# Kernel optimization log

Hardware: AMD Instinct MI355X
Metric: run time of the kernel (lower is better)

Reference implementation:

```python
import jax, jax.numpy as jnp
import numpy as np

T, B = 128, 256          # frames, batch (free dims)
C_IN = 201               # in_features
KD = 3                   # keypoint_dimensionality
NK = C_IN // KD          # 67 keypoints = attention seq len
E = 8                    # d_pose_embed
H = 2                    # heads
DH = E // H              # head dim = 4
L = 12                   # encoder layers
FF = 2 * E               # 16
OUT = 128                # output_size
EPS = 1e-5


def setup_inputs() -> dict:
    key = jax.random.key(0)
    ks = jax.random.split(key, 12)
    s = 0.1
    return {
        "pose_clip": jax.random.normal(ks[0], (T, B, C_IN), jnp.float32),
        "embed_w": jax.random.normal(ks[1], (E, KD), jnp.float32) * s,
        "embed_b": jax.random.normal(ks[2], (E,), jnp.float32) * s,
        "in_proj_w": jax.random.normal(ks[3], (L, 3 * E, E), jnp.float32) * s,
        "in_proj_b": jax.random.normal(ks[4], (L, 3 * E), jnp.float32) * s,
        "attn_out_w": jax.random.normal(ks[5], (L, E, E), jnp.float32) * s,
        "attn_out_b": jax.random.normal(ks[6], (L, E), jnp.float32) * s,
        "ff1_w": jax.random.normal(ks[7], (L, FF, E), jnp.float32) * s,
        "ff1_b": jax.random.normal(ks[8], (L, FF), jnp.float32) * s,
        "ff2_w": jax.random.normal(ks[9], (L, E, FF), jnp.float32) * s,
        "ff2_b": jax.random.normal(ks[10], (L, E), jnp.float32) * s,
        "ln1_g": jnp.ones((L, E), jnp.float32),
        "ln1_b": jnp.zeros((L, E), jnp.float32),
        "ln2_g": jnp.ones((L, E), jnp.float32),
        "ln2_b": jnp.zeros((L, E), jnp.float32),
        "out_w": jax.random.normal(ks[11], (OUT, NK * E), jnp.float32) * s,
        "out_b": jnp.zeros((OUT,), jnp.float32),
    }


def _ln(x, g, b):
    m = jnp.mean(x, axis=-1, keepdims=True)
    v = jnp.mean(jnp.square(x - m), axis=-1, keepdims=True)
    return (x - m) * jax.lax.rsqrt(v + EPS) * g + b


def _encoder(x, layer_params):
    # x: [S, N, E]; post-LN TransformerEncoderLayer, relu activation, no dropout (eval)
    def step(h, p):
        ipw, ipb, aow, aob, f1w, f1b, f2w, f2b, g1, b1, g2, b2 = p
        S, N, _ = h.shape
        qkv = h @ ipw.T + ipb                      # [S, N, 3E]
        q, k, v = jnp.split(qkv, 3, axis=-1)
        q = q.reshape(S, N, H, DH)
        k = k.reshape(S, N, H, DH)
        v = v.reshape(S, N, H, DH)
        scores = jnp.einsum('snhd,tnhd->nhst', q, k) / np.sqrt(DH).astype(h.dtype)
        attn = jax.nn.softmax(scores, axis=-1)
        o = jnp.einsum('nhst,tnhd->snhd', attn, v).reshape(S, N, E)
        o = o @ aow.T + aob
        h = _ln(h + o, g1, b1)
        ff = jax.nn.relu(h @ f1w.T + f1b) @ f2w.T + f2b
        h = _ln(h + ff, g2, b2)
        return h, None
    x, _ = jax.lax.scan(step, x, layer_params)
    return x


def reference(pose_clip, embed_w, embed_b, in_proj_w, in_proj_b, attn_out_w,
              attn_out_b, ff1_w, ff1_b, ff2_w, ff2_b, ln1_g, ln1_b, ln2_g,
              ln2_b, out_w, out_b):
    t, b, c = pose_clip.shape
    nk = c // KD
    # [t,b,c] -> [t*b, nk, 3] -> [nk, t*b, 3]  (seq=keypoints, batch=t*b)
    x = pose_clip.reshape(t * b, nk, KD).transpose(1, 0, 2)
    x = x @ embed_w.T + embed_b                    # [nk, t*b, E]
    layer_params = (in_proj_w, in_proj_b, attn_out_w, attn_out_b,
                    ff1_w, ff1_b, ff2_w, ff2_b, ln1_g, ln1_b, ln2_g, ln2_b)
    x = _encoder(x, layer_params)
    x = x.transpose(1, 0, 2).reshape(t, b, nk * E)  # [t, b, 536]
    return jnp.tanh(x @ out_w.T + out_b)            # [t, b, 128]
```

## Files before the change

kernel.cpp:

```cpp
#include <hip/hip_runtime.h>
#include <math.h>

#define NTOT 32768
#define CIN  201
#define S    67
#define E    8
#define H    2
#define L    12
#define FF   16
#define OUTC 128
#define KF   536
#define EPB  7
#define LPE  34
#define THREADS 256
#define NPAIR 34

typedef float v2f __attribute__((ext_vector_type(2)));

#if __has_builtin(__builtin_amdgcn_exp2f)
#define EXP2F(x) __builtin_amdgcn_exp2f(x)
#else
#define EXP2F(x) exp2f(x)
#endif
#if __has_builtin(__builtin_amdgcn_rcpf)
#define RCPF(x) __builtin_amdgcn_rcpf(x)
#else
#define RCPF(x) (1.0f/(x))
#endif
#if __has_builtin(__builtin_amdgcn_rsqf)
#define RSQF(x) __builtin_amdgcn_rsqf(x)
#else
#define RSQF(x) rsqrtf(x)
#endif

#define QSCALE 0.7213475204444817f

__device__ __forceinline__ v2f sp(float x) { return (v2f){x, x}; }

__device__ __forceinline__ void ln8p(v2f* x, const float* __restrict__ gg,
                                     const float* __restrict__ bb) {
    v2f m = {0.f, 0.f};
    #pragma unroll
    for (int e = 0; e < E; ++e) m += x[e];
    m *= 0.125f;
    v2f v = {0.f, 0.f};
    #pragma unroll
    for (int e = 0; e < E; ++e) { v2f d = x[e] - m; v += d * d; }
    v *= 0.125f;
    v2f rs;
    rs.x = RSQF(v.x + 1e-5f);
    rs.y = RSQF(v.y + 1e-5f);
    #pragma unroll
    for (int e = 0; e < E; ++e) x[e] = (x[e] - m) * rs * sp(gg[e]) + sp(bb[e]);
}

__global__ __launch_bounds__(THREADS, 5)
void enc_kernel(const float* __restrict__ pose,
                const float* __restrict__ ew,  const float* __restrict__ ebias,
                const float* __restrict__ ipw, const float* __restrict__ ipb,
                const float* __restrict__ aow, const float* __restrict__ aob,
                const float* __restrict__ f1w, const float* __restrict__ f1b,
                const float* __restrict__ f2w, const float* __restrict__ f2b,
                const float* __restrict__ g1,  const float* __restrict__ b1,
                const float* __restrict__ g2,  const float* __restrict__ b2,
                float* __restrict__ xf)
{
    __shared__ float4 KA[EPB * H][NPAIR];
    __shared__ float4 KB[EPB * H][NPAIR];
    __shared__ float4 VA[EPB * H][NPAIR];
    __shared__ float4 VB[EPB * H][NPAIR];

    const int lid = threadIdx.x;
    const int g   = lid / LPE;
    const int j   = lid - g * LPE;
    const int n   = blockIdx.x * EPB + g;
    const bool active = (g < EPB) && (n < NTOT);
    const bool pad = (j == LPE - 1);
    const int r0 = 2 * j;

    v2f xr[E];
    if (active) {
        const float* p0 = pose + (size_t)n * CIN + 3 * r0;
        const float* p1 = pad ? p0 : (p0 + 3);
        v2f c0 = {p0[0], p1[0]};
        v2f c1 = {p0[1], p1[1]};
        v2f c2 = {p0[2], p1[2]};
        #pragma unroll
        for (int e = 0; e < E; ++e)
            xr[e] = sp(ebias[e]) + c0 * sp(ew[e*3+0]) + c1 * sp(ew[e*3+1])
                                 + c2 * sp(ew[e*3+2]);
    }

    #pragma unroll 1
    for (int l = 0; l < L; ++l) {
        const float* W  = ipw + l * 192;
        const float* Bq = ipb + l * 24;

        v2f qp[E];
        if (active) {
            v2f qkv[24];
            #pragma unroll
            for (int jo = 0; jo < 24; ++jo) {
                v2f a = sp(Bq[jo]);
                #pragma unroll
                for (int e = 0; e < E; ++e) a += xr[e] * sp(W[jo*8 + e]);
                qkv[jo] = a;
            }
            #pragma unroll
            for (int c = 0; c < E; ++c) qp[c] = qkv[c] * QSCALE;
            if (pad) {
                #pragma unroll
                for (int c = 8; c < 24; ++c) qkv[c].y = 0.f;
            }
            #pragma unroll
            for (int h = 0; h < H; ++h) {
                const int gh = g*2 + h;
                KA[gh][j] = make_float4(qkv[8+4*h+0].x, qkv[8+4*h+0].y,
                                        qkv[8+4*h+1].x, qkv[8+4*h+1].y);
                KB[gh][j] = make_float4(qkv[8+4*h+2].x, qkv[8+4*h+2].y,
                                        qkv[8+4*h+3].x, qkv[8+4*h+3].y);
                VA[gh][j] = make_float4(qkv[16+4*h+0].x, qkv[16+4*h+0].y,
                                        qkv[16+4*h+1].x, qkv[16+4*h+1].y);
                VB[gh][j] = make_float4(qkv[16+4*h+2].x, qkv[16+4*h+2].y,
                                        qkv[16+4*h+3].x, qkv[16+4*h+3].y);
            }
        }
        __syncthreads();

        if (active) {
            v2f os[E];
            #pragma unroll
            for (int h = 0; h < H; ++h) {
                const int gh = g*2 + h;
                const float4* pKA = KA[gh];
                const float4* pKB = KB[gh];
                const float4* pVA = VA[gh];
                const float4* pVB = VB[gh];
                const v2f q0l = sp(qp[4*h+0].x), q0h = sp(qp[4*h+0].y);
                const v2f q1l = sp(qp[4*h+1].x), q1h = sp(qp[4*h+1].y);
                const v2f q2l = sp(qp[4*h+2].x), q2h = sp(qp[4*h+2].y);
                const v2f q3l = sp(qp[4*h+3].x), q3h = sp(qp[4*h+3].y);
                v2f ls0 = {0.f,0.f}, ls1 = {0.f,0.f};
                v2f oc00={0.f,0.f}, oc01={0.f,0.f}, oc02={0.f,0.f}, oc03={0.f,0.f};
                v2f oc10={0.f,0.f}, oc11={0.f,0.f}, oc12={0.f,0.f}, oc13={0.f,0.f};
                #pragma unroll
                for (int i = 0; i < NPAIR; ++i) {
                    float4 ka = pKA[i], kb = pKB[i];
                    float4 va = pVA[i], vb = pVB[i];
                    v2f kx = *(const v2f*)&ka.x, ky = *(const v2f*)&ka.z;
                    v2f kz = *(const v2f*)&kb.x, kw = *(const v2f*)&kb.z;
                    v2f sc0 = q0l*kx + q1l*ky + q2l*kz + q3l*kw;
                    v2f sc1 = q0h*kx + q1h*ky + q2h*kz + q3h*kw;
                    v2f e0, e1;
                    e0.x = EXP2F(sc0.x);  e0.y = EXP2F(sc0.y);
                    e1.x = EXP2F(sc1.x);  e1.y = EXP2F(sc1.y);
                    ls0 += e0;  ls1 += e1;
                    v2f v0 = *(const v2f*)&va.x, v1 = *(const v2f*)&va.z;
                    v2f v2 = *(const v2f*)&vb.x, v3 = *(const v2f*)&vb.z;
                    oc00 += e0*v0; oc01 += e0*v1; oc02 += e0*v2; oc03 += e0*v3;
                    oc10 += e1*v0; oc11 += e1*v1; oc12 += e1*v2; oc13 += e1*v3;
                }
                float l0 = ls0.x + ls0.y - 1.0f;
                float l1 = ls1.x + ls1.y - 1.0f;
                float i0 = RCPF(l0), i1 = RCPF(l1);
                os[4*h+0] = (v2f){(oc00.x+oc00.y)*i0, (oc10.x+oc10.y)*i1};
                os[4*h+1] = (v2f){(oc01.x+oc01.y)*i0, (oc11.x+oc11.y)*i1};
                os[4*h+2] = (v2f){(oc02.x+oc02.y)*i0, (oc12.x+oc12.y)*i1};
                os[4*h+3] = (v2f){(oc03.x+oc03.y)*i0, (oc13.x+oc13.y)*i1};
            }

            {
                const float* WA = aow + l*64;
                const float* BA = aob + l*8;
                #pragma unroll
                for (int e = 0; e < E; ++e) {
                    v2f a = sp(BA[e]);
                    #pragma unroll
                    for (int e2 = 0; e2 < E; ++e2) a += os[e2] * sp(WA[e*8 + e2]);
                    xr[e] += a;
                }
            }
            ln8p(xr, g1 + l*E, b1 + l*E);

            {
                const float* W1 = f1w + l*128;
                const float* B1 = f1b + l*16;
                const float* W2 = f2w + l*128;
                const float* B2 = f2b + l*8;
                v2f t1[FF];
                #pragma unroll
                for (int f = 0; f < FF; ++f) {
                    v2f a = sp(B1[f]);
                    #pragma unroll
                    for (int e = 0; e < E; ++e) a += xr[e] * sp(W1[f*8 + e]);
                    a.x = fmaxf(a.x, 0.f);
                    a.y = fmaxf(a.y, 0.f);
                    t1[f] = a;
                }
                #pragma unroll
                for (int e = 0; e < E; ++e) {
                    v2f a = sp(B2[e]);
                    #pragma unroll
                    for (int f = 0; f < FF; ++f) a += t1[f] * sp(W2[e*16 + f]);
                    xr[e] += a;
                }
            }
            ln8p(xr, g2 + l*E, b2 + l*E);
        }
        __syncthreads();
    }

    if (active) {
        float* dst = xf + (size_t)n * KF + r0 * E;
        *(float4*)(dst + 0) = make_float4(xr[0].x, xr[1].x, xr[2].x, xr[3].x);
        *(float4*)(dst + 4) = make_float4(xr[4].x, xr[5].x, xr[6].x, xr[7].x);
        if (!pad) {
            *(float4*)(dst + 8)  = make_float4(xr[0].y, xr[1].y, xr[2].y, xr[3].y);
            *(float4*)(dst + 12) = make_float4(xr[4].y, xr[5].y, xr[6].y, xr[7].y);
        }
    }
}

__global__ void tr_kernel(const float* __restrict__ ow, float* __restrict__ wt)
{
    int i = blockIdx.x * 256 + threadIdx.x;
    if (i < OUTC * KF) {
        int c = i / KF, k = i - c * KF;
        wt[k * OUTC + c] = ow[i];
    }
}

__global__ __launch_bounds__(256, 4)
void out_kernel(const float* __restrict__ xf, const float* __restrict__ wt,
                const float* __restrict__ ob, float* __restrict__ out)
{
    __shared__ float Xs[32][68];
    const int lid = threadIdx.x;
    const int tx  = lid & 31;
    const int ty  = lid >> 5;
    const int n0  = blockIdx.x * 32;

    float acc[4][4] = {};

    #pragma unroll 1
    for (int kc = 0; kc < 9; ++kc) {
        const int kb = kc * 64;
        const int kw = (kc < 8) ? 64 : 24;
        __syncthreads();
        const int nvec = 32 * (kw >> 2);
        for (int i = lid; i < nvec; i += 256) {
            int r = i / (kw >> 2), kq = i - r * (kw >> 2);
            *(float4*)&Xs[r][kq*4] =
                *(const float4*)&xf[(size_t)(n0 + r) * KF + kb + kq*4];
        }
        __syncthreads();
        #pragma unroll 4
        for (int k = 0; k < kw; ++k) {
            float4 w4 = *(const float4*)&wt[(size_t)(kb + k) * OUTC + tx*4];
            #pragma unroll
            for (int i = 0; i < 4; ++i) {
                float x = Xs[ty*4 + i][k];
                acc[i][0] += x*w4.x; acc[i][1] += x*w4.y;
                acc[i][2] += x*w4.z; acc[i][3] += x*w4.w;
            }
        }
    }

    const float4 bb = *(const float4*)&ob[tx*4];
    #pragma unroll
    for (int i = 0; i < 4; ++i) {
        int r = n0 + ty*4 + i;
        float4 v;
        v.x = tanhf(acc[i][0] + bb.x);
        v.y = tanhf(acc[i][1] + bb.y);
        v.z = tanhf(acc[i][2] + bb.z);
        v.w = tanhf(acc[i][3] + bb.w);
        *(float4*)(out + (size_t)r * OUTC + tx*4) = v;
    }
}

extern "C" void kernel_launch(void* const* d_in, const int* in_sizes, int n_in,
                              void* d_out, int out_size, void* d_ws, size_t ws_size,
                              hipStream_t stream) {
    (void)in_sizes; (void)n_in; (void)out_size; (void)ws_size;
    const float* pose = (const float*)d_in[0];
    const float* ew   = (const float*)d_in[1];
    const float* eb   = (const float*)d_in[2];
    const float* ipw  = (const float*)d_in[3];
    const float* ipb  = (const float*)d_in[4];
    const float* aow  = (const float*)d_in[5];
    const float* aob  = (const float*)d_in[6];
    const float* f1w  = (const float*)d_in[7];
    const float* f1b  = (const float*)d_in[8];
    const float* f2w  = (const float*)d_in[9];
    const float* f2b  = (const float*)d_in[10];
    const float* g1   = (const float*)d_in[11];
    const float* b1   = (const float*)d_in[12];
    const float* g2   = (const float*)d_in[13];
    const float* b2   = (const float*)d_in[14];
    const float* ow   = (const float*)d_in[15];
    const float* ob   = (const float*)d_in[16];

    float* xf = (float*)d_ws;
    float* wt = xf + (size_t)NTOT * KF;

    const int grid1 = (NTOT + EPB - 1) / EPB;
    enc_kernel<<<grid1, THREADS, 0, stream>>>(pose, ew, eb, ipw, ipb, aow, aob,
                                              f1w, f1b, f2w, f2b, g1, b1, g2, b2, xf);
    tr_kernel<<<(OUTC*KF + 255)/256, 256, 0, stream>>>(ow, wt);
    out_kernel<<<NTOT / 32, 256, 0, stream>>>(xf, wt, ob, (float*)d_out);
}
```

Measured before the change: 1.355 ms.

## Rewrite encoder on fp16 MFMA with one wavefront per sequence

Replaces the scalar packed-fp32 encoder with a version that maps each batch element to one wavefront and performs all projections, attention scores, P·V and FFN as 16x16x32 fp16 MFMA ops. A new pack kernel pre-converts per-layer weights to fp16 with the softmax scale folded in. Softmax row sums come from extra ones columns in the V operand, and layernorm uses shuffle reductions. This trades scalar FMA throughput for matrix cores but adds fp16 precision loss, lots of zero padding work and LDS round-trips. Note wpk aliases wt, which tr_kernel overwrites after enc_kernel runs, so the ordering is fine.

```diff
diff --git a/kernel.cpp b/kernel.cpp
--- a/kernel.cpp
+++ b/kernel.cpp
@@ -3,220 +3,311 @@
 
 #define NTOT 32768
 #define CIN  201
-#define S    67
+#define SEQ  67
 #define E    8
-#define H    2
 #define L    12
-#define FF   16
 #define OUTC 128
 #define KF   536
-#define EPB  7
-#define LPE  34
-#define THREADS 256
-#define NPAIR 34
-
-typedef float v2f __attribute__((ext_vector_type(2)));
-
-#if __has_builtin(__builtin_amdgcn_exp2f)
-#define EXP2F(x) __builtin_amdgcn_exp2f(x)
-#else
-#define EXP2F(x) exp2f(x)
-#endif
-#if __has_builtin(__builtin_amdgcn_rcpf)
-#define RCPF(x) __builtin_amdgcn_rcpf(x)
-#else
-#define RCPF(x) (1.0f/(x))
-#endif
-#if __has_builtin(__builtin_amdgcn_rsqf)
-#define RSQF(x) __builtin_amdgcn_rsqf(x)
-#else
-#define RSQF(x) rsqrtf(x)
-#endif
-
-#define QSCALE 0.7213475204444817f
-
-__device__ __forceinline__ v2f sp(float x) { return (v2f){x, x}; }
-
-__device__ __forceinline__ void ln8p(v2f* x, const float* __restrict__ gg,
-                                     const float* __restrict__ bb) {
-    v2f m = {0.f, 0.f};
-    #pragma unroll
-    for (int e = 0; e < E; ++e) m += x[e];
-    m *= 0.125f;
-    v2f v = {0.f, 0.f};
-    #pragma unroll
-    for (int e = 0; e < E; ++e) { v2f d = x[e] - m; v += d * d; }
-    v *= 0.125f;
-    v2f rs;
-    rs.x = RSQF(v.x + 1e-5f);
-    rs.y = RSQF(v.y + 1e-5f);
-    #pragma unroll
-    for (int e = 0; e < E; ++e) x[e] = (x[e] - m) * rs * sp(gg[e]) + sp(bb[e]);
-}
-
-__global__ __launch_bounds__(THREADS, 5)
+#define PWL  512
+
+#define QS 0.7213475204444817f
+
+typedef float f32x4 __attribute__((ext_vector_type(4)));
+typedef __fp16 h8v  __attribute__((ext_vector_type(8)));
+typedef unsigned int u32x4 __attribute__((ext_vector_type(4)));
+typedef unsigned int u32x2 __attribute__((ext_vector_type(2)));
+
+#define MFMA16x16x32 __builtin_amdgcn_mfma_f32_16x16x32_f16
+
+__device__ __forceinline__ h8v  bch8(u32x4 u) { return __builtin_bit_cast(h8v, u); }
+__device__ __forceinline__ u32x4 bcu4(h8v h)  { return __builtin_bit_cast(u32x4, h); }
+__device__ __forceinline__ unsigned pkh(float a, float b) {
+    return __builtin_bit_cast(unsigned, __builtin_amdgcn_cvt_pkrtz(a, b));
+}
+
+
+__global__ void pack_kernel(const float* __restrict__ ipw, const float* __restrict__ ipb,
+                            const float* __restrict__ aow, const float* __restrict__ aob,
+                            const float* __restrict__ f1w, const float* __restrict__ f1b,
+                            const float* __restrict__ f2w, const float* __restrict__ f2b,
+                            const float* __restrict__ g1,  const float* __restrict__ b1,
+                            const float* __restrict__ g2,  const float* __restrict__ b2,
+                            float* __restrict__ wpk)
+{
+    const int l = blockIdx.x, t = threadIdx.x;
+    float* D = wpk + l * PWL;
+    float v = 0.f;
+    if (t < 64) {
+        int o = t >> 2, d = t & 3;
+        float s = (o < 8) ? QS : 1.f;
+        v = __builtin_bit_cast(float, pkh(ipw[l*192 + o*8 + 2*d] * s,
+                                          ipw[l*192 + o*8 + 2*d + 1] * s));
+    } else if (t < 128) {
+        int i = t - 64, cc = i >> 2, d = i & 3;
+        if (cc < 8)
+            v = __builtin_bit_cast(float, pkh(ipw[l*192 + (16+cc)*8 + 2*d],
+                                              ipw[l*192 + (16+cc)*8 + 2*d + 1]));
+    } else if (t < 192) {
+        int i = t - 128, cc = i >> 2, d = i & 3;
+        if (cc < 8)
+            v = __builtin_bit_cast(float, pkh(aow[l*64 + cc*8 + 2*d],
+                                              aow[l*64 + cc*8 + 2*d + 1]));
+    } else if (t < 256) {
+        int i = t - 192, f = i >> 2, d = i & 3;
+        v = __builtin_bit_cast(float, pkh(f1w[l*128 + f*8 + 2*d],
+                                          f1w[l*128 + f*8 + 2*d + 1]));
+    } else if (t < 384) {
+        int i = t - 256, l32 = i >> 2, d = i & 3;
+        int gq = l32 >> 4, cc = l32 & 15;
+        int k = gq*8 + 2*d;
+        if (cc < 8)
+            v = __builtin_bit_cast(float, pkh(f2w[l*128 + cc*16 + k],
+                                              f2w[l*128 + cc*16 + k + 1]));
+    }
+    else if (t < 408) { int j = t-384; v = ipb[l*24 + j] * ((j < 8) ? QS : 1.f); }
+    else if (t < 416) { v = aob[l*8 + (t-408)]; }
+    else if (t < 432) { v = f1b[l*16 + (t-416)]; }
+    else if (t < 440) { v = f2b[l*8 + (t-432)]; }
+    else if (t < 448) { v = g1[l*8 + (t-440)]; }
+    else if (t < 456) { v = b1[l*8 + (t-448)]; }
+    else if (t < 464) { v = g2[l*8 + (t-456)]; }
+    else if (t < 472) { v = b2[l*8 + (t-464)]; }
+    D[t] = v;
+}
+
+#define WSLICE 5888
+
+__global__ __launch_bounds__(256, 2)
 void enc_kernel(const float* __restrict__ pose,
-                const float* __restrict__ ew,  const float* __restrict__ ebias,
-                const float* __restrict__ ipw, const float* __restrict__ ipb,
-                const float* __restrict__ aow, const float* __restrict__ aob,
-                const float* __restrict__ f1w, const float* __restrict__ f1b,
-                const float* __restrict__ f2w, const float* __restrict__ f2b,
-                const float* __restrict__ g1,  const float* __restrict__ b1,
-                const float* __restrict__ g2,  const float* __restrict__ b2,
+                const float* __restrict__ ew, const float* __restrict__ ebias,
+                const float* __restrict__ wpk,
                 float* __restrict__ xf)
 {
-    __shared__ float4 KA[EPB * H][NPAIR];
-    __shared__ float4 KB[EPB * H][NPAIR];
-    __shared__ float4 VA[EPB * H][NPAIR];
-    __shared__ float4 VB[EPB * H][NPAIR];
-
-    const int lid = threadIdx.x;
-    const int g   = lid / LPE;
-    const int j   = lid - g * LPE;
-    const int n   = blockIdx.x * EPB + g;
-    const bool active = (g < EPB) && (n < NTOT);
-    const bool pad = (j == LPE - 1);
-    const int r0 = 2 * j;
-
-    v2f xr[E];
-    if (active) {
-        const float* p0 = pose + (size_t)n * CIN + 3 * r0;
-        const float* p1 = pad ? p0 : (p0 + 3);
-        v2f c0 = {p0[0], p1[0]};
-        v2f c1 = {p0[1], p1[1]};
-        v2f c2 = {p0[2], p1[2]};
-        #pragma unroll
-        for (int e = 0; e < E; ++e)
-            xr[e] = sp(ebias[e]) + c0 * sp(ew[e*3+0]) + c1 * sp(ew[e*3+1])
-                                 + c2 * sp(ew[e*3+2]);
+    __shared__ __fp16 lds[4 * WSLICE];
+    const int lid = threadIdx.x & 63;
+    const int wv  = threadIdx.x >> 6;
+    const int g   = lid >> 4;
+    const int c   = lid & 15;
+    const int n   = blockIdx.x * 4 + wv;
+
+    __fp16* XA = lds + wv * WSLICE;
+    __fp16* QA = XA + 1280;
+    __fp16* KB = QA + 640;
+    __fp16* VT = KB + 640;
+    __fp16* PL = VT + 640;
+
+    const h8v zero8 = bch8((u32x4){0u,0u,0u,0u});
+    const unsigned ONE2 = 0x3C003C00u;
+    const h8v ones8 = bch8((u32x4){ONE2,ONE2,ONE2,ONE2});
+
+    f32x4 xc[5];
+    #pragma unroll
+    for (int si = 0; si < 5; ++si) {
+        f32x4 v = {0.f,0.f,0.f,0.f};
+        if (c < 8) {
+            #pragma unroll
+            for (int rr = 0; rr < 4; ++rr) {
+                int s = si*16 + g*4 + rr;
+                if (s < SEQ) {
+                    const float* p = pose + (size_t)n*CIN + 3*s;
+                    v[rr] = ebias[c] + p[0]*ew[c*3] + p[1]*ew[c*3+1]
+                                     + p[2]*ew[c*3+2];
+                }
+            }
+            #pragma unroll
+            for (int rr = 0; rr < 4; ++rr)
+                XA[(si*16 + g*4 + rr)*16 + c] = (__fp16)v[rr];
+        }
+        xc[si] = v;
     }
 
     #pragma unroll 1
     for (int l = 0; l < L; ++l) {
-        const float* W  = ipw + l * 192;
-        const float* Bq = ipb + l * 24;
-
-        v2f qp[E];
-        if (active) {
-            v2f qkv[24];
-            #pragma unroll
-            for (int jo = 0; jo < 24; ++jo) {
-                v2f a = sp(Bq[jo]);
-                #pragma unroll
-                for (int e = 0; e < E; ++e) a += xr[e] * sp(W[jo*8 + e]);
-                qkv[jo] = a;
-            }
-            #pragma unroll
-            for (int c = 0; c < E; ++c) qp[c] = qkv[c] * QSCALE;
-            if (pad) {
-                #pragma unroll
-                for (int c = 8; c < 24; ++c) qkv[c].y = 0.f;
-            }
-            #pragma unroll
-            for (int h = 0; h < H; ++h) {
-                const int gh = g*2 + h;
-                KA[gh][j] = make_float4(qkv[8+4*h+0].x, qkv[8+4*h+0].y,
-                                        qkv[8+4*h+1].x, qkv[8+4*h+1].y);
-                KB[gh][j] = make_float4(qkv[8+4*h+2].x, qkv[8+4*h+2].y,
-                                        qkv[8+4*h+3].x, qkv[8+4*h+3].y);
-                VA[gh][j] = make_float4(qkv[16+4*h+0].x, qkv[16+4*h+0].y,
-                                        qkv[16+4*h+1].x, qkv[16+4*h+1].y);
-                VB[gh][j] = make_float4(qkv[16+4*h+2].x, qkv[16+4*h+2].y,
-                                        qkv[16+4*h+3].x, qkv[16+4*h+3].y);
-            }
-        }
-        __syncthreads();
-
-        if (active) {
-            v2f os[E];
-            #pragma unroll
-            for (int h = 0; h < H; ++h) {
-                const int gh = g*2 + h;
-                const float4* pKA = KA[gh];
-                const float4* pKB = KB[gh];
-                const float4* pVA = VA[gh];
-                const float4* pVB = VB[gh];
-                const v2f q0l = sp(qp[4*h+0].x), q0h = sp(qp[4*h+0].y);
-                const v2f q1l = sp(qp[4*h+1].x), q1h = sp(qp[4*h+1].y);
-                const v2f q2l = sp(qp[4*h+2].x), q2h = sp(qp[4*h+2].y);
-                const v2f q3l = sp(qp[4*h+3].x), q3h = sp(qp[4*h+3].y);
-                v2f ls0 = {0.f,0.f}, ls1 = {0.f,0.f};
-                v2f oc00={0.f,0.f}, oc01={0.f,0.f}, oc02={0.f,0.f}, oc03={0.f,0.f};
-                v2f oc10={0.f,0.f}, oc11={0.f,0.f}, oc12={0.f,0.f}, oc13={0.f,0.f};
-                #pragma unroll
-                for (int i = 0; i < NPAIR; ++i) {
-                    float4 ka = pKA[i], kb = pKB[i];
-                    float4 va = pVA[i], vb = pVB[i];
-                    v2f kx = *(const v2f*)&ka.x, ky = *(const v2f*)&ka.z;
-                    v2f kz = *(const v2f*)&kb.x, kw = *(const v2f*)&kb.z;
-                    v2f sc0 = q0l*kx + q1l*ky + q2l*kz + q3l*kw;
-                    v2f sc1 = q0h*kx + q1h*ky + q2h*kz + q3h*kw;
-                    v2f e0, e1;
-                    e0.x = EXP2F(sc0.x);  e0.y = EXP2F(sc0.y);
-                    e1.x = EXP2F(sc1.x);  e1.y = EXP2F(sc1.y);
-                    ls0 += e0;  ls1 += e1;
-                    v2f v0 = *(const v2f*)&va.x, v1 = *(const v2f*)&va.z;
-                    v2f v2 = *(const v2f*)&vb.x, v3 = *(const v2f*)&vb.z;
-                    oc00 += e0*v0; oc01 += e0*v1; oc02 += e0*v2; oc03 += e0*v3;
-                    oc10 += e1*v0; oc11 += e1*v1; oc12 += e1*v2; oc13 += e1*v3;
+        const float* PW = wpk + l * PWL;
+
+        h8v wq0 = (g==0) ? *(const h8v*)(PW +   0 + c*4) : zero8;
+        h8v wq1 = (g==0) ? *(const h8v*)(PW +  64 + c*4) : zero8;
+        h8v wao = (g==0) ? *(const h8v*)(PW + 128 + c*4) : zero8;
+        h8v wf1 = (g==0) ? *(const h8v*)(PW + 192 + c*4) : zero8;
+        h8v wf2 = (g< 2) ? *(const h8v*)(PW + 256 + (g*16 + c)*4) : zero8;
+        float bq0 = PW[384 + c];
+        float bq1 = (c<8) ? PW[400 + c] : 0.f;
+        float bao = (c<8) ? PW[408 + c] : 0.f;
+        float bf1 = PW[416 + c];
+        float bf2 = (c<8) ? PW[432 + c] : 0.f;
+        float g1c = (c<8) ? PW[440 + c] : 0.f;
+        float b1c = (c<8) ? PW[448 + c] : 0.f;
+        float g2c = (c<8) ? PW[456 + c] : 0.f;
+        float b2c = (c<8) ? PW[464 + c] : 0.f;
+
+        #pragma unroll
+        for (int si = 0; si < 5; ++si) {
+            h8v af = (g==0) ? *(const h8v*)&XA[(si*16 + c)*16] : zero8;
+            f32x4 c0 = {bq0,bq0,bq0,bq0};
+            f32x4 c1 = {bq1,bq1,bq1,bq1};
+            c0 = MFMA16x16x32(af, wq0, c0, 0,0,0);
+            c1 = MFMA16x16x32(af, wq1, c1, 0,0,0);
+            #pragma unroll
+            for (int rr = 0; rr < 4; ++rr) {
+                int s = si*16 + g*4 + rr;
+                if (c < 8) QA[s*8 + c]       = (__fp16)c0[rr];
+                else       KB[s*8 + (c-8)]   = (__fp16)c0[rr];
+            }
+            if (c < 8) {
+                u32x2 vp;
+                vp.x = pkh(c1[0], c1[1]);
+                vp.y = pkh(c1[2], c1[3]);
+                *(u32x2*)&VT[c*80 + si*16 + g*4] = vp;
+            }
+        }
+
+        h8v qf[5], kbr[5], vb[5];
+        #pragma unroll
+        for (int tj = 0; tj < 5; ++tj) {
+            qf[tj]  = (g==0) ? *(const h8v*)&QA[(tj*16 + c)*8] : zero8;
+            kbr[tj] = (g==0) ? *(const h8v*)&KB[(tj*16 + c)*8] : zero8;
+        }
+        #pragma unroll
+        for (int ch = 0; ch < 5; ++ch) {
+            int tb = ch*32 + g*8;
+            int hb = (tb >= 80) ? 1 : 0;
+            int t0 = tb - hb*80;
+            h8v v = zero8;
+            if (c < 8) {
+                if ((c >> 2) == hb) v = *(const h8v*)&VT[c*80 + t0];
+            } else if (c == 8) {
+                if (!hb) v = ones8;
+            } else if (c == 9) {
+                if (hb)  v = ones8;
+            }
+            vb[ch] = v;
+        }
+
+        #pragma unroll
+        for (int si = 0; si < 5; ++si) {
+            #pragma unroll
+            for (int h = 0; h < 2; ++h) {
+                #pragma unroll
+                for (int tj = 0; tj < 5; ++tj) {
+                    u32x4 kr = bcu4(kbr[tj]);
+                    h8v kf = h ? bch8((u32x4){0u,0u,kr.z,kr.w})
+                               : bch8((u32x4){kr.x,kr.y,0u,0u});
+                    f32x4 sc = {0.f,0.f,0.f,0.f};
+                    sc = MFMA16x16x32(qf[si], kf, sc, 0,0,0);
+                    #pragma unroll
+                    for (int rr = 0; rr < 4; ++rr) {
+                        float e = __builtin_amdgcn_exp2f(sc[rr]);
+                        if (tj == 4 && c >= 3) e = 0.f;
+                        PL[(g*4 + rr)*168 + h*80 + tj*16 + c] = (__fp16)e;
+                    }
                 }
-                float l0 = ls0.x + ls0.y - 1.0f;
-                float l1 = ls1.x + ls1.y - 1.0f;
-                float i0 = RCPF(l0), i1 = RCPF(l1);
-                os[4*h+0] = (v2f){(oc00.x+oc00.y)*i0, (oc10.x+oc10.y)*i1};
-                os[4*h+1] = (v2f){(oc01.x+oc01.y)*i0, (oc11.x+oc11.y)*i1};
-                os[4*h+2] = (v2f){(oc02.x+oc02.y)*i0, (oc12.x+oc12.y)*i1};
-                os[4*h+3] = (v2f){(oc03.x+oc03.y)*i0, (oc13.x+oc13.y)*i1};
-            }
-
-            {
-                const float* WA = aow + l*64;
-                const float* BA = aob + l*8;
-                #pragma unroll
-                for (int e = 0; e < E; ++e) {
-                    v2f a = sp(BA[e]);
-                    #pragma unroll
-                    for (int e2 = 0; e2 < E; ++e2) a += os[e2] * sp(WA[e*8 + e2]);
-                    xr[e] += a;
+            }
+            f32x4 o = {0.f,0.f,0.f,0.f};
+            #pragma unroll
+            for (int ch = 0; ch < 5; ++ch) {
+                h8v pa = *(const h8v*)&PL[c*168 + ch*32 + g*8];
+                o = MFMA16x16x32(pa, vb[ch], o, 0,0,0);
+            }
+            int src = (lid & 48) | (8 + (c >> 2));
+            #pragma unroll
+            for (int rr = 0; rr < 4; ++rr) {
+                float rs = __shfl(o[rr], src, 64);
+                o[rr] *= __builtin_amdgcn_rcpf(rs);
+            }
+            if (c < 8) {
+                #pragma unroll
+                for (int rr = 0; rr < 4; ++rr)
+                    XA[(si*16 + g*4 + rr)*16 + c] = (__fp16)o[rr];
+            }
+        }
+
+        #pragma unroll
+        for (int si = 0; si < 5; ++si) {
+            h8v oaf = (g==0) ? *(const h8v*)&XA[(si*16 + c)*16] : zero8;
+            f32x4 a = {bao,bao,bao,bao};
+            a = MFMA16x16x32(oaf, wao, a, 0,0,0);
+            xc[si] += a;
+        }
+        #pragma unroll
+        for (int si = 0; si < 5; ++si) {
+            f32x4 X = xc[si];
+            f32x4 sx = X, sq = X*X;
+            #pragma unroll
+            for (int m = 1; m <= 4; m <<= 1) {
+                #pragma unroll
+                for (int rr = 0; rr < 4; ++rr) {
+                    sx[rr] += __shfl_xor(sx[rr], m, 64);
+                    sq[rr] += __shfl_xor(sq[rr], m, 64);
                 }
             }
-            ln8p(xr, g1 + l*E, b1 + l*E);
-
-            {
-                const float* W1 = f1w + l*128;
-                const float* B1 = f1b + l*16;
-                const float* W2 = f2w + l*128;
-                const float* B2 = f2b + l*8;
-                v2f t1[FF];
-                #pragma unroll
-                for (int f = 0; f < FF; ++f) {
-                    v2f a = sp(B1[f]);
-                    #pragma unroll
-                    for (int e = 0; e < E; ++e) a += xr[e] * sp(W1[f*8 + e]);
-                    a.x = fmaxf(a.x, 0.f);
-                    a.y = fmaxf(a.y, 0.f);
-                    t1[f] = a;
+            #pragma unroll
+            for (int rr = 0; rr < 4; ++rr) {
+                float mean = sx[rr] * 0.125f;
+                float var  = sq[rr] * 0.125f - mean*mean;
+                float rs   = __builtin_amdgcn_rsqf(var + 1e-5f);
+                float y    = (X[rr] - mean) * rs * g1c + b1c;
+                if (c < 8) X[rr] = y;
+            }
+            xc[si] = X;
+            if (c < 8) {
+                #pragma unroll
+                for (int rr = 0; rr < 4; ++rr)
+                    XA[(si*16 + g*4 + rr)*16 + c] = (__fp16)X[rr];
+            }
+        }
+
+        #pragma unroll
+        for (int si = 0; si < 5; ++si) {
+            h8v xaf = (g==0) ? *(const h8v*)&XA[(si*16 + c)*16] : zero8;
+            f32x4 t = {bf1,bf1,bf1,bf1};
+            t = MFMA16x16x32(xaf, wf1, t, 0,0,0);
+            #pragma unroll
+            for (int rr = 0; rr < 4; ++rr)
+                XA[(si*16 + g*4 + rr)*16 + c] = (__fp16)fmaxf(t[rr], 0.f);
+        }
+        #pragma unroll
+        for (int si = 0; si < 5; ++si) {
+            h8v tf = (g<2) ? *(const h8v*)&XA[(si*16 + c)*16 + g*8] : zero8;
+            f32x4 a = {bf2,bf2,bf2,bf2};
+            a = MFMA16x16x32(tf, wf2, a, 0,0,0);
+            xc[si] += a;
+        }
+        #pragma unroll
+        for (int si = 0; si < 5; ++si) {
+            f32x4 X = xc[si];
+            f32x4 sx = X, sq = X*X;
+            #pragma unroll
+            for (int m = 1; m <= 4; m <<= 1) {
+                #pragma unroll
+                for (int rr = 0; rr < 4; ++rr) {
+                    sx[rr] += __shfl_xor(sx[rr], m, 64);
+                    sq[rr] += __shfl_xor(sq[rr], m, 64);
                 }
-                #pragma unroll
-                for (int e = 0; e < E; ++e) {
-                    v2f a = sp(B2[e]);
-                    #pragma unroll
-                    for (int f = 0; f < FF; ++f) a += t1[f] * sp(W2[e*16 + f]);
-                    xr[e] += a;
-                }
-            }
-            ln8p(xr, g2 + l*E, b2 + l*E);
-        }
-        __syncthreads();
-    }
-
-    if (active) {
-        float* dst = xf + (size_t)n * KF + r0 * E;
-        *(float4*)(dst + 0) = make_float4(xr[0].x, xr[1].x, xr[2].x, xr[3].x);
-        *(float4*)(dst + 4) = make_float4(xr[4].x, xr[5].x, xr[6].x, xr[7].x);
-        if (!pad) {
-            *(float4*)(dst + 8)  = make_float4(xr[0].y, xr[1].y, xr[2].y, xr[3].y);
-            *(float4*)(dst + 12) = make_float4(xr[4].y, xr[5].y, xr[6].y, xr[7].y);
+            }
+            #pragma unroll
+            for (int rr = 0; rr < 4; ++rr) {
+                float mean = sx[rr] * 0.125f;
+                float var  = sq[rr] * 0.125f - mean*mean;
+                float rs   = __builtin_amdgcn_rsqf(var + 1e-5f);
+                float y    = (X[rr] - mean) * rs * g2c + b2c;
+                if (c < 8) X[rr] = y;
+            }
+            xc[si] = X;
+            if (c < 8) {
+                #pragma unroll
+                for (int rr = 0; rr < 4; ++rr)
+                    XA[(si*16 + g*4 + rr)*16 + c] = (__fp16)X[rr];
+            }
+        }
+    }
+
+    #pragma unroll
+    for (int si = 0; si < 5; ++si) {
+        #pragma unroll
+        for (int rr = 0; rr < 4; ++rr) {
+            int s = si*16 + g*4 + rr;
+            if (c < 8 && s < SEQ)
+                xf[(size_t)n*KF + s*8 + c] = xc[si][rr];
         }
     }
 }
@@ -301,12 +392,13 @@
     const float* ow   = (const float*)d_in[15];
     const float* ob   = (const float*)d_in[16];
 
-    float* xf = (float*)d_ws;
-    float* wt = xf + (size_t)NTOT * KF;
-
-    const int grid1 = (NTOT + EPB - 1) / EPB;
-    enc_kernel<<<grid1, THREADS, 0, stream>>>(pose, ew, eb, ipw, ipb, aow, aob,
-                                              f1w, f1b, f2w, f2b, g1, b1, g2, b2, xf);
+    float* xf  = (float*)d_ws;
+    float* wt  = xf + (size_t)NTOT * KF;
+    float* wpk = wt;
+
+    pack_kernel<<<L, 512, 0, stream>>>(ipw, ipb, aow, aob, f1w, f1b, f2w, f2b,
+                                       g1, b1, g2, b2, wpk);
+    enc_kernel<<<NTOT / 4, 256, 0, stream>>>(pose, ew, eb, wpk, xf);
     tr_kernel<<<(OUTC*KF + 255)/256, 256, 0, stream>>>(ow, wt);
     out_kernel<<<NTOT / 32, 256, 0, stream>>>(xf, wt, ob, (float*)d_out);
 }
```

After: 2.652 ms. 95.7% more time.
